# Kernel tuning notes

Hardware: AMD Instinct MI355X
Metric: run time of the kernel (lower is better)

The kernel has to match this reference:

```python
import jax, jax.numpy as jnp
import numpy as np

N_HEAD = 16
CHUNK_SIZE = 64
TOP_B = 8
LOCAL_WINDOW = 256


def _l2_normalize(x, eps=1e-12):
    # matches torch F.normalize(dim=-1): x / max(||x||, eps)
    n = jnp.sqrt(jnp.sum(x * x, axis=-1, keepdims=True))
    return x / jnp.maximum(n, eps)


def setup_inputs() -> dict:
    key = jax.random.key(0)
    ks = jax.random.split(key, 9)
    B, T, C = 2, 2048, 1024
    s = lambda fan_in: 1.0 / np.sqrt(fan_in)
    return {
        "x": jax.random.normal(ks[0], (B, T, C), jnp.float32),
        "Wqkv": jax.random.normal(ks[1], (C, 3 * C), jnp.float32) * s(C),
        "bqkv": jax.random.normal(ks[2], (3 * C,), jnp.float32) * 0.02,
        "Wproj": jax.random.normal(ks[3], (C, C), jnp.float32) * s(C),
        "bproj": jax.random.normal(ks[4], (C,), jnp.float32) * 0.02,
        "Wrouter": jax.random.normal(ks[5], (C, 32), jnp.float32) * s(C),
        "brouter": jax.random.normal(ks[6], (32,), jnp.float32) * 0.02,
        "Wq_rt": jax.random.normal(ks[7], (C, 32), jnp.float32) * s(C),
        "bq_rt": jax.random.normal(ks[8], (32,), jnp.float32) * 0.02,
    }


def reference(x, Wqkv, bqkv, Wproj, bproj, Wrouter, brouter, Wq_rt, bq_rt):
    B, T, C = x.shape
    H = N_HEAD
    D = C // H

    # --- qkv projection ---
    qkv = x @ Wqkv + bqkv                       # [B,T,3C]
    q, k, v = jnp.split(qkv, 3, axis=-1)
    q = q.reshape(B, T, H, D).transpose(0, 2, 1, 3)  # [B,H,T,D]
    k = k.reshape(B, T, H, D).transpose(0, 2, 1, 3)
    v = v.reshape(B, T, H, D).transpose(0, 2, 1, 3)

    # --- routing (T > local_window + chunk_size) ---
    num_chunks = T // CHUNK_SIZE                 # T divisible -> no padding, mask all-True
    chunk_means = x.reshape(B, num_chunks, CHUNK_SIZE, C).mean(axis=2)  # [B,N,C]
    routing_embeds = chunk_means @ Wrouter + brouter                     # [B,N,32]
    q_rt = _l2_normalize(x @ Wq_rt + bq_rt)                              # [B,T,32]
    re_n = _l2_normalize(routing_embeds)
    routing_scores = jnp.einsum('btd,bnd->btn', q_rt, re_n)              # [B,T,N]
    _, chunk_indices = jax.lax.top_k(routing_scores, TOP_B)              # [B,T,top_b]

    # --- dense causal attention (forward path uses is_causal SDPA) ---
    scale = 1.0 / jnp.sqrt(jnp.asarray(D, x.dtype))
    scores = jnp.einsum('bhqd,bhkd->bhqk', q, k) * scale                 # [B,H,T,T]
    causal = jnp.tril(jnp.ones((T, T), dtype=bool))
    scores = jnp.where(causal[None, None], scores, -jnp.inf)
    attn = jax.nn.softmax(scores, axis=-1)
    y = jnp.einsum('bhqk,bhkd->bhqd', attn, v)                           # [B,H,T,D]
    y = y.transpose(0, 2, 1, 3).reshape(B, T, C)
    y = y @ Wproj + bproj

    return y, chunk_indices, routing_scores, routing_embeds
```

## Files before the change

kernel.cpp:

```cpp
#include <hip/hip_runtime.h>
#include <hip/hip_bf16.h>
#include <math.h>

#define B_   2
#define T_   2048
#define C_   1024
#define H_   16
#define D_   64
#define NCH  32
#define RD   32
#define TOPB 8

typedef __attribute__((ext_vector_type(8))) short bf16x8;
typedef __attribute__((ext_vector_type(4))) float f32x4;

static __device__ __forceinline__ unsigned short f2b(float f) {
    return __bfloat16_as_ushort(__float2bfloat16(f));
}

#define SCALE2 0.18033688f

__global__ __launch_bounds__(256) void prep_fused(
    const float* __restrict__ x, unsigned short* __restrict__ xb,
    const float* __restrict__ Wqkv, unsigned short* __restrict__ Wqt,
    const float* __restrict__ Wproj, unsigned short* __restrict__ Wpt,
    const float* __restrict__ Wq_rt, const float* __restrict__ bq_rt,
    float* __restrict__ qrt, float* __restrict__ cm)
{
    __shared__ float smem[64 * 65];
    const int bid = blockIdx.x;
    const int tid = threadIdx.x;

    if (bid < 2048) {
        const int i = bid * 256 + tid;
        float4 a = ((const float4*)x)[i * 2];
        float4 b = ((const float4*)x)[i * 2 + 1];
        bf16x8 o;
        o[0] = (short)f2b(a.x); o[1] = (short)f2b(a.y);
        o[2] = (short)f2b(a.z); o[3] = (short)f2b(a.w);
        o[4] = (short)f2b(b.x); o[5] = (short)f2b(b.y);
        o[6] = (short)f2b(b.z); o[7] = (short)f2b(b.w);
        *(bf16x8*)&xb[(size_t)i * 8] = o;
    } else if (bid < 3072) {
        const float* W; unsigned short* Wt; int N, local;
        if (bid < 2816) { W = Wqkv;  Wt = Wqt; N = 3072; local = bid - 2048; }
        else            { W = Wproj; Wt = Wpt; N = 1024; local = bid - 2816; }
        const int nblk = N >> 6;
        const int n0 = (local % nblk) * 64, k0 = (local / nblk) * 64;
        float (*t)[65] = (float(*)[65])smem;
#pragma unroll
        for (int i = 0; i < 4; i++) {
            const int f = tid + i * 256;
            const int r = f >> 4, c4 = (f & 15) * 4;
            float4 v = *(const float4*)&W[(size_t)(k0 + r) * N + n0 + c4];
            t[r][c4 + 0] = v.x; t[r][c4 + 1] = v.y;
            t[r][c4 + 2] = v.z; t[r][c4 + 3] = v.w;
        }
        __syncthreads();
#pragma unroll
        for (int i = 0; i < 2; i++) {
            const int s = tid + i * 256;
            const int rn = s >> 3, ck8 = (s & 7) * 8;
            bf16x8 o;
#pragma unroll
            for (int j = 0; j < 8; j++) o[j] = (short)f2b(t[ck8 + j][rn]);
            *(bf16x8*)&Wt[(size_t)(n0 + rn) * 1024 + k0 + ck8] = o;
        }
    } else if (bid < 4096) {
        float (*part)[4][32] = (float(*)[4][32])smem;
        const int r0 = (bid - 3072) * 4;
        const int g = tid >> 5;
        const int n = tid & 31;
        const float* w  = Wq_rt + (size_t)(g * 128) * RD + n;
        const float* a0 = x + (size_t)(r0 + 0) * C_ + g * 128;
        const float* a1 = x + (size_t)(r0 + 1) * C_ + g * 128;
        const float* a2 = x + (size_t)(r0 + 2) * C_ + g * 128;
        const float* a3 = x + (size_t)(r0 + 3) * C_ + g * 128;
        float acc0 = 0.f, acc1 = 0.f, acc2 = 0.f, acc3 = 0.f;
#pragma unroll 8
        for (int i = 0; i < 128; i += 4) {
            const float w0 = w[(i + 0) * RD];
            const float w1 = w[(i + 1) * RD];
            const float w2 = w[(i + 2) * RD];
            const float w3 = w[(i + 3) * RD];
            float4 x0 = *(const float4*)&a0[i];
            float4 x1 = *(const float4*)&a1[i];
            float4 x2 = *(const float4*)&a2[i];
            float4 x3 = *(const float4*)&a3[i];
            acc0 += x0.x * w0; acc0 += x0.y * w1; acc0 += x0.z * w2; acc0 += x0.w * w3;
            acc1 += x1.x * w0; acc1 += x1.y * w1; acc1 += x1.z * w2; acc1 += x1.w * w3;
            acc2 += x2.x * w0; acc2 += x2.y * w1; acc2 += x2.z * w2; acc2 += x2.w * w3;
            acc3 += x3.x * w0; acc3 += x3.y * w1; acc3 += x3.z * w2; acc3 += x3.w * w3;
        }
        part[g][0][n] = acc0;
        part[g][1][n] = acc1;
        part[g][2][n] = acc2;
        part[g][3][n] = acc3;
        __syncthreads();
        if (g < 4) {
            float s = part[0][g][n];
#pragma unroll
            for (int gg = 1; gg < 8; gg++) s += part[gg][g][n];
            s += bq_rt[n];
            float ss = s * s;
#pragma unroll
            for (int off = 16; off >= 1; off >>= 1) ss += __shfl_xor(ss, off, 32);
            qrt[(size_t)(r0 + g) * RD + n] = s / fmaxf(sqrtf(ss), 1e-12f);
        }
    } else {
        const int local = bid - 4096;
        const int bc = local & 63;
        const int b = bc >> 5, n = bc & 31;
        const int c = (local >> 6) * 256 + tid;
        const float* xp = x + ((size_t)b * T_ + n * 64) * C_;
        float s = 0.f;
        for (int i = 0; i < 64; i++) s += xp[(size_t)i * C_ + c];
        cm[(size_t)bc * C_ + c] = s * (1.0f / 64.0f);
    }
}

__global__ void embeds_kernel(const float* __restrict__ cm, const float* __restrict__ W,
                              const float* __restrict__ bias,
                              float* __restrict__ emb_out, float* __restrict__ ren)
{
    const int row  = blockIdx.x * 8 + (threadIdx.x >> 5);
    const int lane = threadIdx.x & 31;
    if (row >= B_ * NCH) return;
    const float* a = cm + (size_t)row * C_;
    float acc = 0.f;
    for (int k = 0; k < C_; k += 4) {
        float4 a4 = *(const float4*)&a[k];
        acc += a4.x * W[(k + 0) * RD + lane];
        acc += a4.y * W[(k + 1) * RD + lane];
        acc += a4.z * W[(k + 2) * RD + lane];
        acc += a4.w * W[(k + 3) * RD + lane];
    }
    acc += bias[lane];
    emb_out[(size_t)row * RD + lane] = acc;
    float ss = acc * acc;
#pragma unroll
    for (int off = 16; off >= 1; off >>= 1) ss += __shfl_xor(ss, off, 32);
    ren[(size_t)row * RD + lane] = acc / fmaxf(sqrtf(ss), 1e-12f);
}

__global__ __launch_bounds__(512, 1) void gemm_qkv_256(
    const unsigned short* __restrict__ A, const unsigned short* __restrict__ Bt,
    const float* __restrict__ bias,
    unsigned short* __restrict__ qp, unsigned short* __restrict__ kp,
    unsigned short* __restrict__ vp, int M, int N, int K)
{
    __shared__ unsigned short lds[3][2][8192];

    const int tid  = threadIdx.x;
    const int wid  = tid >> 6;
    const int lane = tid & 63;
    const int lr = lane & 15, lg = lane >> 4;
    const int wm = wid >> 2, wn = wid & 3;

    const int bid = blockIdx.x;
    const int swz = (bid & 7) * 24 + (bid >> 3);
    const int m0 = (swz & 15) << 8;
    const int n0 = (swz >> 4) << 8;

    const int srow = tid >> 2;
    const int sswz = (((srow & 3) ^ ((srow >> 2) & 3)) << 4);
    const int skel = (((tid & 3) << 4) ^ sswz) >> 1;
    const unsigned short* gA0 = A  + (size_t)(m0 + srow) * K + skel;
    const unsigned short* gA1 = A  + (size_t)(m0 + srow + 128) * K + skel;
    const unsigned short* gB0 = Bt + (size_t)(n0 + srow) * K + skel;
    const unsigned short* gB1 = Bt + (size_t)(n0 + srow + 128) * K + skel;
    const int lb0 = (wid * 64) * 8;
    const int lb1 = (wid * 64 + 512) * 8;

#define QSTAGE(sl, kofs)                                                          \
    __builtin_amdgcn_global_load_lds(                                             \
        (const __attribute__((address_space(1))) int*)(gA0 + (kofs)),             \
        (__attribute__((address_space(3))) int*)&lds[sl][0][lb0], 16, 0, 0);      \
    __builtin_amdgcn_global_load_lds(                                             \
        (const __attribute__((address_space(1))) int*)(gA1 + (kofs)),             \
        (__attribute__((address_space(3))) int*)&lds[sl][0][lb1], 16, 0, 0);      \
    __builtin_amdgcn_global_load_lds(                                             \
        (const __attribute__((address_space(1))) int*)(gB0 + (kofs)),             \
        (__attribute__((address_space(3))) int*)&lds[sl][1][lb0], 16, 0, 0);      \
    __builtin_amdgcn_global_load_lds(                                             \
        (const __attribute__((address_space(1))) int*)(gB1 + (kofs)),             \
        (__attribute__((address_space(3))) int*)&lds[sl][1][lb1], 16, 0, 0);

    const int rswz = (((lr & 3) ^ ((lr >> 2) & 3)) << 4);
    const int acol = (((lg << 4) ^ rswz) >> 1);

    f32x4 acc[8][4];
#pragma unroll
    for (int i = 0; i < 8; i++)
#pragma unroll
        for (int j = 0; j < 4; j++) acc[i][j] = (f32x4){0.f, 0.f, 0.f, 0.f};

    const int nt = K >> 5;

    QSTAGE(0, 0)
    QSTAGE(1, 32)
    asm volatile("s_waitcnt vmcnt(4)" ::: "memory");
    __builtin_amdgcn_s_barrier();

    int cur = 0;
    for (int t = 0; t < nt; ++t) {
        int s2 = cur + 2; if (s2 >= 3) s2 -= 3;
        if (t + 2 < nt) { QSTAGE(s2, (t + 2) << 5) }

        const unsigned short* sA = &lds[cur][0][0];
        const unsigned short* sB = &lds[cur][1][0];

        bf16x8 bfr[4];
#pragma unroll
        for (int ni = 0; ni < 4; ni++)
            bfr[ni] = *(const bf16x8*)&sB[(wn * 64 + ni * 16 + lr) * 32 + acol];

        __builtin_amdgcn_s_setprio(1);
#pragma unroll
        for (int mi = 0; mi < 8; mi++) {
            bf16x8 af = *(const bf16x8*)&sA[(wm * 128 + mi * 16 + lr) * 32 + acol];
#pragma unroll
            for (int ni = 0; ni < 4; ni++)
                acc[mi][ni] = __builtin_amdgcn_mfma_f32_16x16x32_bf16(
                    af, bfr[ni], acc[mi][ni], 0, 0, 0);
        }
        __builtin_amdgcn_s_setprio(0);

        if (t + 1 < nt) {
            if (t + 2 < nt) { asm volatile("s_waitcnt vmcnt(4)" ::: "memory"); }
            else            { asm volatile("s_waitcnt vmcnt(0)" ::: "memory"); }
            __builtin_amdgcn_s_barrier();
        }
        cur += 1; if (cur == 3) cur = 0;
    }
#undef QSTAGE

#pragma unroll
    for (int ni = 0; ni < 4; ni++) {
        const int col = n0 + wn * 64 + ni * 16 + lr;
        const float bv = bias[col];
        const int which = col >> 10;
        const int c  = col & 1023;
        const int hh = c >> 6;
        const int dd = c & 63;
        unsigned short* dst = (which == 0) ? qp : (which == 1) ? kp : vp;
        const float postmul = (which == 0) ? SCALE2 : 1.0f;
#pragma unroll
        for (int mi = 0; mi < 8; mi++) {
#pragma unroll
            for (int r = 0; r < 4; r++) {
                const int row = m0 + wm * 128 + mi * 16 + lg * 4 + r;
                const int bb = row >> 11, tt = row & 2047;
                dst[(((size_t)bb * H_ + hh) * T_ + tt) * D_ + dd] =
                    f2b((acc[mi][ni][r] + bv) * postmul);
            }
        }
    }
}

__global__ __launch_bounds__(256) void gemm_mfma_f32out(
    const unsigned short* __restrict__ A, const unsigned short* __restrict__ Bt,
    const float* __restrict__ bias, float* __restrict__ out, int M, int N, int K)
{
    __shared__ unsigned short As[2][128 * 32];
    __shared__ unsigned short Bs[2][128 * 32];

    const int tid  = threadIdx.x;
    const int lane = tid & 63;
    const int wave = tid >> 6;
    const int lr = lane & 15, lg = lane >> 4;
    const int wm = wave >> 1, wn = wave & 1;
    const int n0 = blockIdx.x * 128, m0 = blockIdx.y * 128;

    const int srow = tid >> 2;
    const int scol = (tid & 3) * 8;
    const unsigned short* ga = A  + (size_t)(m0 + srow) * K + scol;
    const unsigned short* gb = Bt + (size_t)(n0 + srow) * K + scol;
    const int ldst = (tid & 0xC0) * 8;

    f32x4 acc[4][4];
#pragma unroll
    for (int i = 0; i < 4; i++)
#pragma unroll
        for (int j = 0; j < 4; j++) acc[i][j] = (f32x4){0.f, 0.f, 0.f, 0.f};

#define GSTAGE(buf, k0)                                                        \
    _Pragma("unroll")                                                          \
    for (int i = 0; i < 2; i++) {                                              \
        __builtin_amdgcn_global_load_lds(                                      \
            (const __attribute__((address_space(1))) int*)(ga + (k0) + (size_t)i * 64 * K), \
            (__attribute__((address_space(3))) int*)&As[buf][i * 2048 + ldst], 16, 0, 0);   \
        __builtin_amdgcn_global_load_lds(                                      \
            (const __attribute__((address_space(1))) int*)(gb + (k0) + (size_t)i * 64 * K), \
            (__attribute__((address_space(3))) int*)&Bs[buf][i * 2048 + ldst], 16, 0, 0);   \
    }

    const int nt = K >> 5;
    GSTAGE(0, 0);
    __syncthreads();

    int cur = 0;
    for (int t = 0; t < nt; ++t) {
        if (t + 1 < nt) { GSTAGE(cur ^ 1, (t + 1) << 5); }

        bf16x8 af[4], bfr[4];
#pragma unroll
        for (int mi = 0; mi < 4; mi++)
            af[mi] = *(const bf16x8*)&As[cur][(wm * 64 + mi * 16 + lr) * 32 + lg * 8];
#pragma unroll
        for (int ni = 0; ni < 4; ni++)
            bfr[ni] = *(const bf16x8*)&Bs[cur][(wn * 64 + ni * 16 + lr) * 32 + lg * 8];
#pragma unroll
        for (int mi = 0; mi < 4; mi++)
#pragma unroll
            for (int ni = 0; ni < 4; ni++)
                acc[mi][ni] = __builtin_amdgcn_mfma_f32_16x16x32_bf16(
                    af[mi], bfr[ni], acc[mi][ni], 0, 0, 0);

        __syncthreads();
        cur ^= 1;
    }
#undef GSTAGE

#pragma unroll
    for (int ni = 0; ni < 4; ni++) {
        const int col = n0 + wn * 64 + ni * 16 + lr;
        const float bv = bias[col];
#pragma unroll
        for (int mi = 0; mi < 4; mi++) {
#pragma unroll
            for (int r = 0; r < 4; r++) {
                const int row = m0 + wm * 64 + mi * 16 + lg * 4 + r;
                out[(size_t)row * N + col] = acc[mi][ni][r] + bv;
            }
        }
    }
}

__global__ void scores_topk(const float* __restrict__ qrt, const float* __restrict__ ren,
                            float* __restrict__ sc_out, float* __restrict__ idx_out)
{
    const int row = blockIdx.x * 64 + threadIdx.x;
    if (row >= B_ * T_) return;
    const int b = row / T_;
    float q[RD];
#pragma unroll
    for (int i = 0; i < RD; i++) q[i] = qrt[(size_t)row * RD + i];
    const float* rb = ren + (size_t)b * NCH * RD;
    float s[NCH];
#pragma unroll 4
    for (int n = 0; n < NCH; n++) {
        float acc = 0.f;
#pragma unroll
        for (int i = 0; i < RD; i++) acc += q[i] * rb[n * RD + i];
        s[n] = acc;
        sc_out[(size_t)row * NCH + n] = acc;
    }
    unsigned mask = 0;
    for (int t = 0; t < TOPB; t++) {
        float best = -INFINITY;
        int bi = 0;
#pragma unroll
        for (int n = 0; n < NCH; n++) {
            const bool ok = !((mask >> n) & 1u) && (s[n] > best);
            if (ok) { best = s[n]; bi = n; }
        }
        mask |= (1u << bi);
        idx_out[(size_t)row * TOPB + t] = (float)bi;
    }
}

#define LSTR 68

__global__ __launch_bounds__(256) void attn_mfma(
    const unsigned short* __restrict__ qg, const unsigned short* __restrict__ kg,
    const unsigned short* __restrict__ vg, unsigned short* __restrict__ y)
{
    const int bid = blockIdx.x;
    const int xcd = bid & 7;
    const int j   = bid >> 3;
    const int h   = xcd + 8 * (j & 1);
    const int b   = (j >> 1) & 1;
    const int qt  = 31 - (j >> 2);

    const int tid  = threadIdx.x;
    const int wave = tid >> 6;
    const int lane = tid & 63;
    const int lg = lane >> 4;
    const int lr = lane & 15;

    __shared__ short Ks[2][64][LSTR];
    __shared__ short Vt[2][64][LSTR];

    const size_t base = ((size_t)(b * H_ + h) * T_) * D_;

    bf16x8 qf0, qf1;
    {
        const short* qp = (const short*)qg + base + (size_t)(qt * 64 + wave * 16 + lr) * D_;
        qf0 = *(const bf16x8*)&qp[lg * 8];
        qf1 = *(const bf16x8*)&qp[32 + lg * 8];
    }

    const int srr = tid >> 2;
    const int sc0 = (tid & 3) * 16;
    const int vrp = tid & 31;
    const int vcg = tid >> 5;
    const int kv0   = 2 * vrp;
    const int vslot = ((kv0 >> 5) << 5) + (((kv0 >> 2) & 3) << 3) +
                      (((kv0 >> 4) & 1) << 2) + (kv0 & 3);

    bf16x8 kreg0, kreg1, vreg0, vreg1;

    float m_run = -INFINITY, l_run = 0.f;
    f32x4 oacc[4];
#pragma unroll
    for (int r = 0; r < 4; r++) oacc[r] = (f32x4){0.f, 0.f, 0.f, 0.f};
    const int qrow_g = qt * 64 + wave * 16 + lr;

#define VPACK(buf)                                                              \
    {                                                                           \
        const unsigned* v0d = (const unsigned*)&vreg0;                          \
        const unsigned* v1d = (const unsigned*)&vreg1;                          \
        _Pragma("unroll")                                                       \
        for (int jj = 0; jj < 8; jj++) {                                        \
            const unsigned sel = (jj & 1) ? 0x07060302u : 0x05040100u;          \
            const unsigned dw = __builtin_amdgcn_perm(v1d[jj >> 1], v0d[jj >> 1], sel); \
            *(unsigned*)&Vt[buf][vcg * 8 + jj][vslot] = dw;                     \
        }                                                                       \
    }

    {
        const short* kp = (const short*)kg + base + (size_t)srr * D_ + sc0;
        kreg0 = *(const bf16x8*)kp;
        kreg1 = *(const bf16x8*)(kp + 8);
        const short* vp = (const short*)vg + base + (size_t)kv0 * D_ + vcg * 8;
        vreg0 = *(const bf16x8*)vp;
        vreg1 = *(const bf16x8*)(vp + D_);
    }
    {
        *(bf16x8*)&Ks[0][srr][sc0]     = kreg0;
        *(bf16x8*)&Ks[0][srr][sc0 + 8] = kreg1;
        VPACK(0)
    }
    if (qt >= 1) {
        const short* kp = (const short*)kg + base + (size_t)(64 + srr) * D_ + sc0;
        kreg0 = *(const bf16x8*)kp;
        kreg1 = *(const bf16x8*)(kp + 8);
        const short* vp = (const short*)vg + base + (size_t)(64 + kv0) * D_ + vcg * 8;
        vreg0 = *(const bf16x8*)vp;
        vreg1 = *(const bf16x8*)(vp + D_);
    }
    __syncthreads();

    for (int kt = 0; kt <= qt; ++kt) {
        const int cur = kt & 1;

        if (kt < qt) {
            *(bf16x8*)&Ks[cur ^ 1][srr][sc0]     = kreg0;
            *(bf16x8*)&Ks[cur ^ 1][srr][sc0 + 8] = kreg1;
            VPACK(cur ^ 1)
        }
        if (kt + 2 <= qt) {
            const short* kp = (const short*)kg + base + (size_t)((kt + 2) * 64 + srr) * D_ + sc0;
            kreg0 = *(const bf16x8*)kp;
            kreg1 = *(const bf16x8*)(kp + 8);
            const short* vp = (const short*)vg + base + (size_t)((kt + 2) * 64 + kv0) * D_ + vcg * 8;
            vreg0 = *(const bf16x8*)vp;
            vreg1 = *(const bf16x8*)(vp + D_);
        }

        f32x4 s[4];
        __builtin_amdgcn_s_setprio(1);
#pragma unroll
        for (int cb = 0; cb < 4; cb++) {
            bf16x8 kf0 = *(const bf16x8*)&Ks[cur][cb * 16 + lr][lg * 8];
            bf16x8 kf1 = *(const bf16x8*)&Ks[cur][cb * 16 + lr][32 + lg * 8];
            f32x4 acc = (f32x4){0.f, 0.f, 0.f, 0.f};
            acc = __builtin_amdgcn_mfma_f32_16x16x32_bf16(kf0, qf0, acc, 0, 0, 0);
            acc = __builtin_amdgcn_mfma_f32_16x16x32_bf16(kf1, qf1, acc, 0, 0, 0);
            s[cb] = acc;
        }
        __builtin_amdgcn_s_setprio(0);

        if (kt == qt) {
#pragma unroll
            for (int cb = 0; cb < 4; cb++)
#pragma unroll
                for (int r = 0; r < 4; r++)
                    if (kt * 64 + cb * 16 + lg * 4 + r > qrow_g) s[cb][r] = -INFINITY;
        }

        float rm;
        {
            const float t0 = fmaxf(fmaxf(s[0][0], s[0][1]), fmaxf(s[0][2], s[0][3]));
            const float t1 = fmaxf(fmaxf(s[1][0], s[1][1]), fmaxf(s[1][2], s[1][3]));
            const float t2 = fmaxf(fmaxf(s[2][0], s[2][1]), fmaxf(s[2][2], s[2][3]));
            const float t3 = fmaxf(fmaxf(s[3][0], s[3][1]), fmaxf(s[3][2], s[3][3]));
            rm = fmaxf(fmaxf(t0, t1), fmaxf(t2, t3));
        }
        rm = fmaxf(rm, __shfl_xor(rm, 16));
        rm = fmaxf(rm, __shfl_xor(rm, 32));

        if (!__all(rm <= m_run + 8.0f)) {
            const float mnew = fmaxf(m_run, rm);
            const float fsc  = exp2f(m_run - mnew);
            m_run = mnew;
            l_run *= fsc;
            float fr[4];
#pragma unroll
            for (int r = 0; r < 4; r++) fr[r] = __shfl(fsc, lg * 4 + r);
#pragma unroll
            for (int db = 0; db < 4; db++)
#pragma unroll
                for (int r = 0; r < 4; r++) oacc[db][r] *= fr[r];
        }

        float p[4][4];
#pragma unroll
        for (int cb = 0; cb < 4; cb++)
#pragma unroll
            for (int r = 0; r < 4; r++)
                p[cb][r] = exp2f(s[cb][r] - m_run);
        float rs;
        {
            const float t0 = (p[0][0] + p[0][1]) + (p[0][2] + p[0][3]);
            const float t1 = (p[1][0] + p[1][1]) + (p[1][2] + p[1][3]);
            const float t2 = (p[2][0] + p[2][1]) + (p[2][2] + p[2][3]);
            const float t3 = (p[3][0] + p[3][1]) + (p[3][2] + p[3][3]);
            rs = (t0 + t1) + (t2 + t3);
        }
        rs += __shfl_xor(rs, 16);
        rs += __shfl_xor(rs, 32);
        l_run += rs;

        bf16x8 pf0, pf1;
#pragma unroll
        for (int r = 0; r < 4; r++) {
            pf0[r]     = (short)f2b(p[0][r]);
            pf0[4 + r] = (short)f2b(p[1][r]);
            pf1[r]     = (short)f2b(p[2][r]);
            pf1[4 + r] = (short)f2b(p[3][r]);
        }

        __builtin_amdgcn_s_setprio(1);
#pragma unroll
        for (int db = 0; db < 4; db++) {
            bf16x8 vf0 = *(const bf16x8*)&Vt[cur][db * 16 + lr][lg * 8];
            bf16x8 vf1 = *(const bf16x8*)&Vt[cur][db * 16 + lr][32 + lg * 8];
            oacc[db] = __builtin_amdgcn_mfma_f32_16x16x32_bf16(pf0, vf0, oacc[db], 0, 0, 0);
            oacc[db] = __builtin_amdgcn_mfma_f32_16x16x32_bf16(pf1, vf1, oacc[db], 0, 0, 0);
        }
        __builtin_amdgcn_s_setprio(0);

        __syncthreads();
    }
#undef VPACK

#pragma unroll
    for (int r = 0; r < 4; r++) {
        const float lrow = __shfl(l_run, lg * 4 + r);
        const float inv = 1.0f / lrow;
        const int trow = qt * 64 + wave * 16 + lg * 4 + r;
        unsigned short* yp = y + (size_t)(b * T_ + trow) * C_ + h * D_;
#pragma unroll
        for (int db = 0; db < 4; db++)
            yp[db * 16 + lr] = f2b(oacc[db][r] * inv);
    }
}

extern "C" void kernel_launch(void* const* d_in, const int* in_sizes, int n_in,
                              void* d_out, int out_size, void* d_ws, size_t ws_size,
                              hipStream_t stream)
{
    const float* x       = (const float*)d_in[0];
    const float* Wqkv    = (const float*)d_in[1];
    const float* bqkv    = (const float*)d_in[2];
    const float* Wproj   = (const float*)d_in[3];
    const float* bproj   = (const float*)d_in[4];
    const float* Wrouter = (const float*)d_in[5];
    const float* brouter = (const float*)d_in[6];
    const float* Wq_rt   = (const float*)d_in[7];
    const float* bq_rt   = (const float*)d_in[8];

    float* out = (float*)d_out;
    char*  ws  = (char*)d_ws;

    const size_t MT  = (size_t)B_ * T_;
    const size_t QKV = MT * C_;

    unsigned short* xb   = (unsigned short*)ws;
    unsigned short* Wqt  = xb  + QKV;
    unsigned short* Wpt  = Wqt + (size_t)3 * C_ * C_;
    unsigned short* q    = Wpt + (size_t)C_ * C_;
    unsigned short* k    = q + QKV;
    unsigned short* v    = k + QKV;
    unsigned short* yab  = v + QKV;
    float* cm   = (float*)(yab + QKV);
    float* qrt  = cm  + (size_t)B_ * NCH * C_;
    float* ren  = qrt + MT * RD;

    float* y_out   = out;
    float* idx_out = out + QKV;
    float* sc_out  = idx_out + MT * TOPB;
    float* emb_out = sc_out + MT * NCH;

    prep_fused<<<4352, 256, 0, stream>>>(x, xb, Wqkv, Wqt, Wproj, Wpt,
                                         Wq_rt, bq_rt, qrt, cm);

    gemm_qkv_256<<<dim3(192), 512, 0, stream>>>(
        xb, Wqt, bqkv, q, k, v, (int)MT, 3 * C_, C_);

    embeds_kernel<<<8, 256, 0, stream>>>(cm, Wrouter, brouter, emb_out, ren);
    scores_topk<<<(int)(MT / 64), 64, 0, stream>>>(qrt, ren, sc_out, idx_out);

    attn_mfma<<<dim3(1024), 256, 0, stream>>>(q, k, v, yab);

    gemm_mfma_f32out<<<dim3(C_ / 128, MT / 128), 256, 0, stream>>>(
        yab, Wpt, bproj, y_out, (int)MT, C_, C_);
}
```

Measured before the change: 186.8 us.

## Triple-buffer and swizzle LDS in projection GEMM; reorder attention tile scheduling

The output projection GEMM moves from double to triple buffering, with direct-to-LDS loads issued two stages ahead and partial vmcnt waits in place of full syncthreads. An XOR swizzle on the LDS layout is meant to remove bank conflicts on fragment reads, and s_setprio raises wave priority around the MFMA block. The attention kernel's block-to-query-tile mapping changes so long and short causal tiles are interleaved, which should balance load across CUs. The risks are extra LDS use, lower occupancy from launch_bounds(256,1), and getting the hand-written wait counts right.

```diff
diff --git a/kernel.cpp b/kernel.cpp
--- a/kernel.cpp
+++ b/kernel.cpp
@@ -258,12 +258,11 @@
     }
 }
 
-__global__ __launch_bounds__(256) void gemm_mfma_f32out(
+__global__ __launch_bounds__(256, 1) void gemm_proj_128(
     const unsigned short* __restrict__ A, const unsigned short* __restrict__ Bt,
     const float* __restrict__ bias, float* __restrict__ out, int M, int N, int K)
 {
-    __shared__ unsigned short As[2][128 * 32];
-    __shared__ unsigned short Bs[2][128 * 32];
+    __shared__ unsigned short lds[3][2][4096];
 
     const int tid  = threadIdx.x;
     const int lane = tid & 63;
@@ -273,10 +272,30 @@
     const int n0 = blockIdx.x * 128, m0 = blockIdx.y * 128;
 
     const int srow = tid >> 2;
-    const int scol = (tid & 3) * 8;
-    const unsigned short* ga = A  + (size_t)(m0 + srow) * K + scol;
-    const unsigned short* gb = Bt + (size_t)(n0 + srow) * K + scol;
-    const int ldst = (tid & 0xC0) * 8;
+    const int sswz = (((srow & 3) ^ ((srow >> 2) & 3)) << 4);
+    const int skel = (((tid & 3) << 4) ^ sswz) >> 1;
+    const unsigned short* gA0 = A  + (size_t)(m0 + srow) * K + skel;
+    const unsigned short* gA1 = A  + (size_t)(m0 + srow + 64) * K + skel;
+    const unsigned short* gB0 = Bt + (size_t)(n0 + srow) * K + skel;
+    const unsigned short* gB1 = Bt + (size_t)(n0 + srow + 64) * K + skel;
+    const int ldb = (tid & 0xC0) * 8;
+
+#define PSTAGE(sl, kofs)                                                          \
+    __builtin_amdgcn_global_load_lds(                                             \
+        (const __attribute__((address_space(1))) int*)(gA0 + (kofs)),             \
+        (__attribute__((address_space(3))) int*)&lds[sl][0][ldb], 16, 0, 0);      \
+    __builtin_amdgcn_global_load_lds(                                             \
+        (const __attribute__((address_space(1))) int*)(gA1 + (kofs)),             \
+        (__attribute__((address_space(3))) int*)&lds[sl][0][2048 + ldb], 16, 0, 0); \
+    __builtin_amdgcn_global_load_lds(                                             \
+        (const __attribute__((address_space(1))) int*)(gB0 + (kofs)),             \
+        (__attribute__((address_space(3))) int*)&lds[sl][1][ldb], 16, 0, 0);      \
+    __builtin_amdgcn_global_load_lds(                                             \
+        (const __attribute__((address_space(1))) int*)(gB1 + (kofs)),             \
+        (__attribute__((address_space(3))) int*)&lds[sl][1][2048 + ldb], 16, 0, 0);
+
+    const int rswz = (((lr & 3) ^ ((lr >> 2) & 3)) << 4);
+    const int acol = (((lg << 4) ^ rswz) >> 1);
 
     f32x4 acc[4][4];
 #pragma unroll
@@ -284,43 +303,46 @@
 #pragma unroll
         for (int j = 0; j < 4; j++) acc[i][j] = (f32x4){0.f, 0.f, 0.f, 0.f};
 
-#define GSTAGE(buf, k0)                                                        \
-    _Pragma("unroll")                                                          \
-    for (int i = 0; i < 2; i++) {                                              \
-        __builtin_amdgcn_global_load_lds(                                      \
-            (const __attribute__((address_space(1))) int*)(ga + (k0) + (size_t)i * 64 * K), \
-            (__attribute__((address_space(3))) int*)&As[buf][i * 2048 + ldst], 16, 0, 0);   \
-        __builtin_amdgcn_global_load_lds(                                      \
-            (const __attribute__((address_space(1))) int*)(gb + (k0) + (size_t)i * 64 * K), \
-            (__attribute__((address_space(3))) int*)&Bs[buf][i * 2048 + ldst], 16, 0, 0);   \
-    }
-
     const int nt = K >> 5;
-    GSTAGE(0, 0);
-    __syncthreads();
+
+    PSTAGE(0, 0)
+    PSTAGE(1, 32)
+    asm volatile("s_waitcnt vmcnt(4)" ::: "memory");
+    __builtin_amdgcn_s_barrier();
 
     int cur = 0;
     for (int t = 0; t < nt; ++t) {
-        if (t + 1 < nt) { GSTAGE(cur ^ 1, (t + 1) << 5); }
+        int s2 = cur + 2; if (s2 >= 3) s2 -= 3;
+        if (t + 2 < nt) { PSTAGE(s2, (t + 2) << 5) }
+
+        const unsigned short* sA = &lds[cur][0][0];
+        const unsigned short* sB = &lds[cur][1][0];
 
         bf16x8 af[4], bfr[4];
 #pragma unroll
         for (int mi = 0; mi < 4; mi++)
-            af[mi] = *(const bf16x8*)&As[cur][(wm * 64 + mi * 16 + lr) * 32 + lg * 8];
+            af[mi] = *(const bf16x8*)&sA[(wm * 64 + mi * 16 + lr) * 32 + acol];
 #pragma unroll
         for (int ni = 0; ni < 4; ni++)
-            bfr[ni] = *(const bf16x8*)&Bs[cur][(wn * 64 + ni * 16 + lr) * 32 + lg * 8];
+            bfr[ni] = *(const bf16x8*)&sB[(wn * 64 + ni * 16 + lr) * 32 + acol];
+
+        __builtin_amdgcn_s_setprio(1);
 #pragma unroll
         for (int mi = 0; mi < 4; mi++)
 #pragma unroll
             for (int ni = 0; ni < 4; ni++)
                 acc[mi][ni] = __builtin_amdgcn_mfma_f32_16x16x32_bf16(
                     af[mi], bfr[ni], acc[mi][ni], 0, 0, 0);
-
-        __syncthreads();
-        cur ^= 1;
-    }
-#undef GSTAGE
+        __builtin_amdgcn_s_setprio(0);
+
+        if (t + 1 < nt) {
+            if (t + 2 < nt) { asm volatile("s_waitcnt vmcnt(4)" ::: "memory"); }
+            else            { asm volatile("s_waitcnt vmcnt(0)" ::: "memory"); }
+            __builtin_amdgcn_s_barrier();
+        }
+        cur += 1; if (cur == 3) cur = 0;
+    }
+#undef PSTAGE
 
 #pragma unroll
     for (int ni = 0; ni < 4; ni++) {
@@ -378,10 +400,10 @@
 {
     const int bid = blockIdx.x;
     const int xcd = bid & 7;
-    const int j   = bid >> 3;
-    const int h   = xcd + 8 * (j & 1);
-    const int b   = (j >> 1) & 1;
-    const int qt  = 31 - (j >> 2);
+    const int h   = xcd + 8 * ((bid >> 3) & 1);
+    const int b   = (bid >> 4) & 1;
+    const int i   = bid >> 5;
+    const int qt  = (i & 8) ? ((i & 16) ? (i - 24) : (i + 8)) : (31 - i);
 
     const int tid  = threadIdx.x;
     const int wave = tid >> 6;
@@ -615,6 +637,6 @@
 
     attn_mfma<<<dim3(1024), 256, 0, stream>>>(q, k, v, yab);
 
-    gemm_mfma_f32out<<<dim3(C_ / 128, MT / 128), 256, 0, stream>>>(
+    gemm_proj_128<<<dim3(C_ / 128, MT / 128), 256, 0, stream>>>(
         yab, Wpt, bproj, y_out, (int)MT, C_, C_);
 }
```

New measurement: 181.7 us. 2.7% less time.
